# Kernel optimization log

Hardware: AMD Instinct MI355X
Metric: run time of the kernel (lower is better)

Reference implementation:

```python
import jax, jax.numpy as jnp
import numpy as np

R, M1, N1, M2, N2 = 4, 1024, 2048, 2, 4
BATCH, SEQ = 4, 2048


def setup_inputs() -> dict:
    key = jax.random.key(0)
    k_x, k_A, k_B, k_b, k_p, k_q = jax.random.split(key, 6)
    x = jax.random.normal(k_x, (BATCH, SEQ, M1 * M2), dtype=jnp.float32)
    A = jax.random.normal(k_A, (R, N1, M1), dtype=jnp.float32) * 0.001
    B = jax.random.normal(k_B, (R, M2, N2), dtype=jnp.float32) * 0.001
    b = jnp.zeros((N1 * N2,), dtype=jnp.float32)
    p_inv = jax.random.permutation(k_p, M1 * M2).astype(jnp.int32)
    q = jax.random.permutation(k_q, N1 * N2).astype(jnp.int32)
    return {"x": x, "A": A, "B": B, "b": b, "p_inv": p_inv, "q": q}


def reference(x, A, B, b, p_inv, q):
    # x: [Bt, S, m1*m2]; A: [r, n1, m1]; B: [r, m2, n2]
    r, n1, m1 = A.shape
    _, m2, n2 = B.shape
    shape = x.shape
    tokens = shape[0] * shape[1]
    # input permutation gather (use_p=True)
    xp = x[:, :, p_inv]
    # Bx = einsum('km,rmn->rkn'): [r, tokens*m1, n2]
    xf = xp.reshape(-1, m2)
    Bx = jnp.einsum('km,rmn->rkn', xf, B)
    Bx = Bx.reshape(r, tokens, m1, n2)
    # ABx = einsum('rnm,rbmj->bnj'): [tokens, n1, n2]
    ABx = jnp.einsum('rnm,rbmj->bnj', A, Bx)
    ABx = ABx.reshape(shape[:-1] + (n1 * n2,))
    # output permutation gather (use_q=True) + bias
    out = ABx[:, :, q] + b
    return out
```

## Files before the change

### kernel.cpp

```cpp
#include <hip/hip_runtime.h>
#include <hip/hip_bf16.h>

typedef unsigned short u16;
typedef __attribute__((ext_vector_type(8))) short short8;
typedef __attribute__((ext_vector_type(4))) float floatx4;

#define TOKENS 8192
#define KDIM   2048
#define NFEAT  8192
#define R_     4
#define N1_    2048
#define M1_    1024

#define BM 256
#define BN 256
#define BK 64
#define NITER (KDIM / (2 * BK))

__device__ __forceinline__ u16 f2bf(float f) {
  union { float f; unsigned u; } v; v.f = f;
  unsigned r = v.u + 0x7fffu + ((v.u >> 16) & 1u);
  return (u16)(r >> 16);
}

__global__ void k_invert_perm(const int* __restrict__ p_inv, int* __restrict__ pf) {
  int i = blockIdx.x * 256 + threadIdx.x;
  if (i < KDIM) pf[p_inv[i]] = i;
}

#define CVT_BLOCKS 16384
struct u16x4 { u16 a, b, c, d; };
__global__ void k_prep(const float4* __restrict__ x4, u16x4* __restrict__ xb,
                       const float* __restrict__ A, const float* __restrict__ Bm,
                       const int* __restrict__ pf, const int* __restrict__ q,
                       u16* __restrict__ Wf) {
  int bid = blockIdx.x;
  if (bid < CVT_BLOCKS) {
    int i = bid * 256 + threadIdx.x;
    float4 v = x4[i];
    u16x4 o; o.a = f2bf(v.x); o.b = f2bf(v.y); o.c = f2bf(v.z); o.d = f2bf(v.w);
    xb[i] = o;
  } else {
    int f = bid - CVT_BLOCKS;
    int k0 = threadIdx.x * 8;
    int qf = q[f];
    int n = qf >> 2, jq = qf & 3;
    const float* An = A + (size_t)n * M1_;
    float bc[8];
#pragma unroll
    for (int r = 0; r < R_; ++r) {
      bc[r * 2 + 0] = Bm[r * 8 + 0 * 4 + jq];
      bc[r * 2 + 1] = Bm[r * 8 + 1 * 4 + jq];
    }
    int4 c0 = *(const int4*)(pf + k0);
    int4 c1 = *(const int4*)(pf + k0 + 4);
    int cs[8] = {c0.x, c0.y, c0.z, c0.w, c1.x, c1.y, c1.z, c1.w};
    u16 w[8];
#pragma unroll
    for (int i = 0; i < 8; ++i) {
      int m1 = cs[i] >> 1, m2 = cs[i] & 1;
      float acc = 0.f;
#pragma unroll
      for (int r = 0; r < R_; ++r)
        acc += An[(size_t)r * (N1_ * M1_) + m1] * bc[r * 2 + m2];
      w[i] = f2bf(acc);
    }
    *(short8*)(Wf + (size_t)f * KDIM + k0) = *(const short8*)w;
  }
}

#define GLD16(gp, lp) __builtin_amdgcn_global_load_lds( \
    (const __attribute__((address_space(1))) void*)(gp), \
    (__attribute__((address_space(3))) void*)(lp), 16, 0, 0)

#define FENCE asm volatile("" ::: "memory")
#define BAR   do { FENCE; __builtin_amdgcn_s_barrier(); FENCE; } while (0)
#define LGKM0 asm volatile("s_waitcnt lgkmcnt(0)" ::: "memory")
#define VMCNT(n) asm volatile("s_waitcnt vmcnt(" #n ")" ::: "memory")

__global__ __launch_bounds__(512, 2) void k_gemm(
    const u16* __restrict__ X, const u16* __restrict__ W,
    const float* __restrict__ bias, float* __restrict__ out) {
  __shared__ __align__(16) char lds[2 * 65536];

  int bid = blockIdx.x;
  int xcd = bid & 7;
  int loc = bid >> 3;
  int u = loc >> 5, v = loc & 31;
  int tM = xcd * 4 + (v >> 3);
  int tN = u * 8 + (v & 7);
  int rowBase = tM * BM, colBase = tN * BN;

  int tid = threadIdx.x, lane = tid & 63, wave = tid >> 6;
  int wm = wave >> 2;
  int wn = wave & 3;

  int srow = tid >> 3;
  int scol = ((tid & 7) ^ (srow & 7)) * 8;
  const u16* Asrc = X + (size_t)(rowBase + srow) * KDIM + scol;
  const u16* Bsrc = W + (size_t)(colBase + srow) * KDIM + scol;

  auto SA = [&](int slot, int half, int kt) {
#pragma unroll
    for (int jj = 0; jj < 2; ++jj)
      GLD16(Asrc + (size_t)(half * 128 + jj * 64) * KDIM + kt * 64,
            &lds[slot * 65536 + half * 16384 + jj * 8192 + tid * 16]);
  };
  auto SB = [&](int slot, int half, int kt) {
#pragma unroll
    for (int jj = 0; jj < 2; ++jj)
      GLD16(Bsrc + (size_t)(half * 128 + jj * 64) * KDIM + kt * 64,
            &lds[slot * 65536 + 32768 + half * 16384 + jj * 8192 + tid * 16]);
  };

  int l15 = lane & 15, lhi = lane >> 4, l7 = lane & 7;
  int x0 = (lhi ^ l7) * 16;
  int x1 = ((4 + lhi) ^ l7) * 16;
  int abase = wm * 16384 + l15 * 128;
  int bbase = 32768 + (wn >> 1) * 16384 + ((wn & 1) * 64 + l15) * 128;

  auto RA = [&](int slot, int m, int kk) -> short8 {
    return *(const short8*)&lds[slot * 65536 + abase + m * 2048 + (kk ? x1 : x0)];
  };
  auto RB = [&](int slot, int n, int kk) -> short8 {
    return *(const short8*)&lds[slot * 65536 + bbase + n * 2048 + (kk ? x1 : x0)];
  };

  floatx4 acc[8][4] = {};
  short8 a[4][2], a2[4][2], b[2][2], b2[2][2];

  auto RDa = [&](int slot) {
#pragma unroll
    for (int m = 0; m < 4; ++m) { a[m][0] = RA(slot, m, 0); a[m][1] = RA(slot, m, 1); }
  };
  auto RDa2 = [&](int slot) {
#pragma unroll
    for (int m = 0; m < 4; ++m) { a2[m][0] = RA(slot, 4 + m, 0); a2[m][1] = RA(slot, 4 + m, 1); }
  };
  auto RDb = [&](int slot) {
#pragma unroll
    for (int n = 0; n < 2; ++n) { b[n][0] = RB(slot, n, 0); b[n][1] = RB(slot, n, 1); }
  };
  auto RDb2 = [&](int slot) {
#pragma unroll
    for (int n = 0; n < 2; ++n) { b2[n][0] = RB(slot, 2 + n, 0); b2[n][1] = RB(slot, 2 + n, 1); }
  };

  auto MM = [&](short8 (&Af)[4][2], short8 (&Bf)[2][2], int mo, int no) {
    __builtin_amdgcn_s_setprio(1);
#pragma unroll
    for (int m = 0; m < 4; ++m)
#pragma unroll
      for (int n = 0; n < 2; ++n) {
        acc[mo + m][no + n] = __builtin_amdgcn_mfma_f32_16x16x32_bf16(Af[m][0], Bf[n][0], acc[mo + m][no + n], 0, 0, 0);
        acc[mo + m][no + n] = __builtin_amdgcn_mfma_f32_16x16x32_bf16(Af[m][1], Bf[n][1], acc[mo + m][no + n], 0, 0, 0);
      }
    __builtin_amdgcn_s_setprio(0);
  };

  SA(0, 0, 0); SA(0, 1, 0); SB(0, 0, 0); SB(0, 1, 0);
  SA(1, 0, 1); SA(1, 1, 1);
  VMCNT(4);
  BAR;
  RDa(0); RDb(0);

  for (int it = 0; it < NITER - 1; ++it) {
    int t0 = 2 * it;
    LGKM0;
    RDa2(0); SB(1, 0, t0 + 1);
    MM(a, b, 0, 0);
    BAR;
    LGKM0;
    RDb2(0); SB(1, 1, t0 + 1);
    MM(a2, b, 4, 0);
    BAR;
    LGKM0;
    SA(0, 0, t0 + 2);
    MM(a2, b2, 4, 2);
    VMCNT(2);
    BAR;
    LGKM0;
    SA(0, 1, t0 + 2);
    MM(a, b2, 0, 2);
    RDa(1); RDb(1);
    BAR;
    LGKM0;
    RDa2(1); SB(0, 0, t0 + 2);
    MM(a, b, 0, 0);
    BAR;
    LGKM0;
    RDb2(1); SB(0, 1, t0 + 2);
    MM(a2, b, 4, 0);
    BAR;
    LGKM0;
    SA(1, 0, t0 + 3);
    MM(a2, b2, 4, 2);
    VMCNT(2);
    BAR;
    LGKM0;
    SA(1, 1, t0 + 3);
    MM(a, b2, 0, 2);
    RDa(0); RDb(0);
    BAR;
  }

  {
    int t0 = 2 * (NITER - 1);
    LGKM0; RDa2(0); SB(1, 0, t0 + 1); MM(a, b, 0, 0); BAR;
    LGKM0; RDb2(0); SB(1, 1, t0 + 1); MM(a2, b, 4, 0); BAR;
    LGKM0; MM(a2, b2, 4, 2); VMCNT(0); BAR;
    LGKM0; MM(a, b2, 0, 2); RDa(1); RDb(1);
    LGKM0; RDa2(1); MM(a, b, 0, 0);
    LGKM0; RDb2(1); MM(a2, b, 4, 0);
    LGKM0; MM(a2, b2, 4, 2);
    MM(a, b2, 0, 2);
  }

  float bv[4];
#pragma unroll
  for (int n = 0; n < 4; ++n)
    bv[n] = bias[colBase + wn * 64 + n * 16 + l15];
#pragma unroll
  for (int m = 0; m < 8; ++m) {
    int r0 = wm * 128 + m * 16 + (lhi << 2);
#pragma unroll
    for (int n = 0; n < 4; ++n) {
      size_t basep = (size_t)(rowBase + r0) * NFEAT + colBase + wn * 64 + n * 16 + l15;
#pragma unroll
      for (int reg = 0; reg < 4; ++reg)
        out[basep + (size_t)reg * NFEAT] = acc[m][n][reg] + bv[n];
    }
  }
}

extern "C" void kernel_launch(void* const* d_in, const int* in_sizes, int n_in,
                              void* d_out, int out_size, void* d_ws, size_t ws_size,
                              hipStream_t stream) {
  const float* x     = (const float*)d_in[0];
  const float* A     = (const float*)d_in[1];
  const float* Bm    = (const float*)d_in[2];
  const float* bias  = (const float*)d_in[3];
  const int*   p_inv = (const int*)d_in[4];
  const int*   q     = (const int*)d_in[5];
  float* out = (float*)d_out;

  u16* Xb = (u16*)d_ws;
  u16* Wf = (u16*)((char*)d_ws + (size_t)TOKENS * KDIM * 2);
  int* pf = (int*)((char*)d_ws + (size_t)TOKENS * KDIM * 2 * 2);

  k_invert_perm<<<(KDIM + 255) / 256, 256, 0, stream>>>(p_inv, pf);
  k_prep<<<CVT_BLOCKS + NFEAT, 256, 0, stream>>>((const float4*)x, (u16x4*)Xb, A, Bm, pf, q, Wf);
  k_gemm<<<(TOKENS / BM) * (NFEAT / BN), 512, 0, stream>>>(Xb, Wf, bias, out);
}
```

Measured before the change: 314.1 us.

## Halve GEMM barriers by batching tile loads, fuse perm inversion into prep

After: 307.0 us. -2.2%, faster.

```diff
diff --git a/kernel.cpp b/kernel.cpp
--- a/kernel.cpp
+++ b/kernel.cpp
@@ -23,17 +23,13 @@
   return (u16)(r >> 16);
 }
 
-__global__ void k_invert_perm(const int* __restrict__ p_inv, int* __restrict__ pf) {
-  int i = blockIdx.x * 256 + threadIdx.x;
-  if (i < KDIM) pf[p_inv[i]] = i;
-}
-
 #define CVT_BLOCKS 16384
 struct u16x4 { u16 a, b, c, d; };
 __global__ void k_prep(const float4* __restrict__ x4, u16x4* __restrict__ xb,
                        const float* __restrict__ A, const float* __restrict__ Bm,
-                       const int* __restrict__ pf, const int* __restrict__ q,
+                       const int* __restrict__ p_inv, const int* __restrict__ q,
                        u16* __restrict__ Wf) {
+  __shared__ int pfs[KDIM];
   int bid = blockIdx.x;
   if (bid < CVT_BLOCKS) {
     int i = bid * 256 + threadIdx.x;
@@ -42,6 +38,8 @@
     xb[i] = o;
   } else {
     int f = bid - CVT_BLOCKS;
+    for (int i = threadIdx.x; i < KDIM; i += 256) pfs[p_inv[i]] = i;
+    __syncthreads();
     int k0 = threadIdx.x * 8;
     int qf = q[f];
     int n = qf >> 2, jq = qf & 3;
@@ -52,13 +50,11 @@
       bc[r * 2 + 0] = Bm[r * 8 + 0 * 4 + jq];
       bc[r * 2 + 1] = Bm[r * 8 + 1 * 4 + jq];
     }
-    int4 c0 = *(const int4*)(pf + k0);
-    int4 c1 = *(const int4*)(pf + k0 + 4);
-    int cs[8] = {c0.x, c0.y, c0.z, c0.w, c1.x, c1.y, c1.z, c1.w};
     u16 w[8];
 #pragma unroll
     for (int i = 0; i < 8; ++i) {
-      int m1 = cs[i] >> 1, m2 = cs[i] & 1;
+      int c = pfs[k0 + i];
+      int m1 = c >> 1, m2 = c & 1;
       float acc = 0.f;
 #pragma unroll
       for (int r = 0; r < R_; ++r)
@@ -159,61 +155,56 @@
   };
 
   SA(0, 0, 0); SA(0, 1, 0); SB(0, 0, 0); SB(0, 1, 0);
-  SA(1, 0, 1); SA(1, 1, 1);
-  VMCNT(4);
+  SA(1, 0, 1); SA(1, 1, 1); SB(1, 0, 1); SB(1, 1, 1);
+  VMCNT(8);
   BAR;
   RDa(0); RDb(0);
 
   for (int it = 0; it < NITER - 1; ++it) {
     int t0 = 2 * it;
-    LGKM0;
-    RDa2(0); SB(1, 0, t0 + 1);
+    LGKM0; RDa2(0);
     MM(a, b, 0, 0);
-    BAR;
-    LGKM0;
-    RDb2(0); SB(1, 1, t0 + 1);
+    FENCE;
+    LGKM0; RDb2(0);
     MM(a2, b, 4, 0);
     BAR;
     LGKM0;
-    SA(0, 0, t0 + 2);
+    SA(0, 0, t0 + 2); SA(0, 1, t0 + 2);
     MM(a2, b2, 4, 2);
-    VMCNT(2);
-    BAR;
-    LGKM0;
-    SA(0, 1, t0 + 2);
+    VMCNT(4);
+    BAR;
+    LGKM0;
+    SB(0, 0, t0 + 2); SB(0, 1, t0 + 2);
     MM(a, b2, 0, 2);
     RDa(1); RDb(1);
-    BAR;
-    LGKM0;
-    RDa2(1); SB(0, 0, t0 + 2);
+    FENCE;
+    LGKM0; RDa2(1);
     MM(a, b, 0, 0);
-    BAR;
-    LGKM0;
-    RDb2(1); SB(0, 1, t0 + 2);
+    FENCE;
+    LGKM0; RDb2(1);
     MM(a2, b, 4, 0);
     BAR;
     LGKM0;
-    SA(1, 0, t0 + 3);
+    SA(1, 0, t0 + 3); SA(1, 1, t0 + 3);
     MM(a2, b2, 4, 2);
-    VMCNT(2);
-    BAR;
-    LGKM0;
-    SA(1, 1, t0 + 3);
+    VMCNT(4);
+    BAR;
+    LGKM0;
+    SB(1, 0, t0 + 3); SB(1, 1, t0 + 3);
     MM(a, b2, 0, 2);
     RDa(0); RDb(0);
-    BAR;
+    FENCE;
   }
 
   {
-    int t0 = 2 * (NITER - 1);
-    LGKM0; RDa2(0); SB(1, 0, t0 + 1); MM(a, b, 0, 0); BAR;
-    LGKM0; RDb2(0); SB(1, 1, t0 + 1); MM(a2, b, 4, 0); BAR;
+    LGKM0; RDa2(0); MM(a, b, 0, 0); FENCE;
+    LGKM0; RDb2(0); MM(a2, b, 4, 0); BAR;
     LGKM0; MM(a2, b2, 4, 2); VMCNT(0); BAR;
-    LGKM0; MM(a, b2, 0, 2); RDa(1); RDb(1);
-    LGKM0; RDa2(1); MM(a, b, 0, 0);
-    LGKM0; RDb2(1); MM(a2, b, 4, 0);
-    LGKM0; MM(a2, b2, 4, 2);
-    MM(a, b2, 0, 2);
+    LGKM0; MM(a, b2, 0, 2); RDa(1); RDb(1); FENCE;
+    LGKM0; RDa2(1); MM(a, b, 0, 0); FENCE;
+    LGKM0; RDb2(1); MM(a2, b, 4, 0); FENCE;
+    LGKM0; MM(a2, b2, 4, 2); FENCE;
+    LGKM0; MM(a, b2, 0, 2);
   }
 
   float bv[4];
@@ -246,9 +237,7 @@
 
   u16* Xb = (u16*)d_ws;
   u16* Wf = (u16*)((char*)d_ws + (size_t)TOKENS * KDIM * 2);
-  int* pf = (int*)((char*)d_ws + (size_t)TOKENS * KDIM * 2 * 2);
-
-  k_invert_perm<<<(KDIM + 255) / 256, 256, 0, stream>>>(p_inv, pf);
-  k_prep<<<CVT_BLOCKS + NFEAT, 256, 0, stream>>>((const float4*)x, (u16x4*)Xb, A, Bm, pf, q, Wf);
+
+  k_prep<<<CVT_BLOCKS + NFEAT, 256, 0, stream>>>((const float4*)x, (u16x4*)Xb, A, Bm, p_inv, q, Wf);
   k_gemm<<<(TOKENS / BM) * (NFEAT / BN), 512, 0, stream>>>(Xb, Wf, bias, out);
 }
```
